# Performance work log

Measured on AMD Instinct MI355X. Metric: run time of the kernel, lower is better.

## Reference

```python
import jax, jax.numpy as jnp
import numpy as np

N = 100000   # nodes
E = 1600000  # edges (avg degree 16)
D = 64       # feature dim
LN_EPS = 1e-5


def setup_inputs() -> dict:
    key = jax.random.key(0)
    ks = jax.random.split(key, 12)
    s = 1.0 / np.sqrt(D)
    x = jax.random.normal(ks[0], (N, D), dtype=jnp.float32)
    edge_index = jax.random.randint(ks[1], (2, E), 0, N, dtype=jnp.int32)
    routing_factor = jax.random.uniform(ks[2], (E,), dtype=jnp.float32)
    return {
        "x": x,
        "edge_index": edge_index,
        "routing_factor": routing_factor,
        "W_phys": jax.random.normal(ks[3], (D, D), dtype=jnp.float32) * s,
        "W_neur": jax.random.normal(ks[4], (D, D), dtype=jnp.float32) * s,
        "att_w": jax.random.normal(ks[5], (2 * D,), dtype=jnp.float32) * s,
        "channel_fusion": jnp.float32(0.5),
        "mlp_w1": jax.random.normal(ks[6], (2 * D, D), dtype=jnp.float32) * s,
        "mlp_b1": jnp.zeros((2 * D,), dtype=jnp.float32),
        "mlp_w2": jax.random.normal(ks[7], (D, 2 * D), dtype=jnp.float32) / np.sqrt(2 * D),
        "mlp_b2": jnp.zeros((D,), dtype=jnp.float32),
        "ln1_g": jnp.ones((D,), dtype=jnp.float32),
        "ln1_b": jnp.zeros((D,), dtype=jnp.float32),
        "ln2_g": jnp.ones((D,), dtype=jnp.float32),
        "ln2_b": jnp.zeros((D,), dtype=jnp.float32),
    }


def _layernorm(h, g, b):
    mu = jnp.mean(h, axis=-1, keepdims=True)
    var = jnp.var(h, axis=-1, keepdims=True)
    return (h - mu) * jax.lax.rsqrt(var + LN_EPS) * g + b


def reference(x, edge_index, routing_factor, W_phys, W_neur, att_w,
              channel_fusion, mlp_w1, mlp_b1, mlp_w2, mlp_b2,
              ln1_g, ln1_b, ln2_g, ln2_b):
    src, dst = edge_index[0], edge_index[1]
    x_src = x[src]  # [E, D]
    # att(cat([x_src, x_dst])) == x_src @ w[:D] + x_dst @ w[D:]
    att_scores = x_src @ att_w[:D] + x[dst] @ att_w[D:]  # [E]
    # segment softmax over destination nodes (equivalent to per-node loop)
    seg_max = jax.ops.segment_max(att_scores, dst, num_segments=N)
    e = jnp.exp(att_scores - seg_max[dst])
    denom = jax.ops.segment_sum(e, dst, num_segments=N)
    att = e / denom[dst]  # [E]
    # dual-channel messages (dropout inactive at eval)
    phys = routing_factor[:, None] * (x_src @ W_phys.T)
    neur = x_src @ W_neur.T
    alpha = jax.nn.sigmoid(channel_fusion)
    messages = att[:, None] * (alpha * phys + (1.0 - alpha) * neur)  # [E, D]
    out = jax.ops.segment_sum(messages, dst, num_segments=N)  # [N, D]
    h = _layernorm(jax.nn.gelu(out, approximate=False) + x, ln1_g, ln1_b)
    m = jax.nn.gelu(h @ mlp_w1.T + mlp_b1, approximate=False) @ mlp_w2.T + mlp_b2
    return _layernorm(m + h, ln2_g, ln2_b)
```

## Files before the change

### kernel.cpp

```cpp
#include <hip/hip_runtime.h>
#include <math.h>

#define NN 100000
#define NE 1600000
#define DD 64
#define NBUK 782
#define TILE 8192
#define NTB ((NE + TILE - 1) / TILE)
#define NWB 96
#define NPB ((NN + 255) / 256)
#define BSTRIDE 3072
#define SCAP 3072

typedef __attribute__((ext_vector_type(8))) short short8;
typedef __attribute__((ext_vector_type(4))) float f32x4;
typedef __attribute__((ext_vector_type(4))) _Float16 h4;
typedef __attribute__((ext_vector_type(2))) _Float16 f16x2;

__device__ __forceinline__ float gelu_exact(float v) {
    return 0.5f * v * (1.0f + erff(v * 0.7071067811865475f));
}

__device__ __forceinline__ unsigned short f2bf(float f) {
    unsigned u = __float_as_uint(f);
    return (unsigned short)((u + 0x7FFFu + ((u >> 16) & 1u)) >> 16);
}
__device__ __forceinline__ float bf2f(unsigned short h) {
    return __uint_as_float((unsigned)h << 16);
}
__device__ __forceinline__ void split8v(float4 x0, float4 x1, short8& hi, short8& lo) {
    float v[8] = {x0.x, x0.y, x0.z, x0.w, x1.x, x1.y, x1.z, x1.w};
    #pragma unroll
    for (int i = 0; i < 8; ++i) {
        unsigned short h = f2bf(v[i]);
        hi[i] = (short)h;
        lo[i] = (short)f2bf(v[i] - bf2f(h));
    }
}
__device__ __forceinline__ void lds_frag(const float* g, int row, int u0, int s,
                                         short8& hi, short8& lo) {
    float4 p0 = *(const float4*)&g[row * 64 + ((u0 ^ s) << 2)];
    float4 p1 = *(const float4*)&g[row * 64 + (((u0 + 1) ^ s) << 2)];
    split8v(p0, p1, hi, lo);
}

__device__ __forceinline__ f16x2 as_f16x2(unsigned int u) {
    union { unsigned int x; f16x2 h; } c; c.x = u; return c.h;
}
__device__ __forceinline__ unsigned short h_as_us(_Float16 h) {
    union { _Float16 h; unsigned short u; } c; c.h = h; return c.u;
}
__device__ __forceinline__ float us_as_f(unsigned short u) {
    union { unsigned short u; _Float16 h; } c; c.u = u; return (float)c.h;
}

__global__ __launch_bounds__(256) void kfront(
    const int* __restrict__ ei, const float* __restrict__ rf,
    int* __restrict__ bcount, uint2* __restrict__ tmp,
    const float* __restrict__ Wp, const float* __restrict__ Wn,
    const float* __restrict__ w1, const float* __restrict__ w2,
    const float* __restrict__ cf,
    unsigned short* __restrict__ wh, unsigned short* __restrict__ wl,
    const float* __restrict__ x, const float* __restrict__ attw,
    float* __restrict__ es1, _Float16* __restrict__ xh)
{
    __shared__ int hist[NBUK];
    __shared__ int gbase[NBUK];
    int bid = blockIdx.x;
    int tid = threadIdx.x;

    if (bid < NTB) {
        for (int i = tid; i < NBUK; i += 256) hist[i] = 0;
        __syncthreads();
        int base = bid * TILE;
        int end  = min(base + TILE, NE);
        for (int e = base + tid; e < end; e += 256)
            atomicAdd(&hist[ei[NE + e] >> 7], 1);
        __syncthreads();
        for (int i = tid; i < NBUK; i += 256) {
            int c = hist[i];
            gbase[i] = c ? (i * BSTRIDE + atomicAdd(bcount + i, c)) : 0;
            hist[i] = 0;
        }
        __syncthreads();
        for (int e0 = base + tid; e0 < end; e0 += 256 * 4) {
            int srcs[4], dsts[4]; unsigned rfs[4];
            #pragma unroll
            for (int q = 0; q < 4; ++q) {
                int e = e0 + q * 256;
                if (e < end) {
                    srcs[q] = ei[e];
                    dsts[q] = ei[NE + e];
                    rfs[q]  = __float_as_uint(rf[e]);
                }
            }
            #pragma unroll
            for (int q = 0; q < 4; ++q) {
                int e = e0 + q * 256;
                if (e < end) {
                    int b = dsts[q] >> 7;
                    int t = atomicAdd(&hist[b], 1);
                    tmp[gbase[b] + t] = make_uint2(
                        (unsigned)srcs[q] | ((unsigned)(dsts[q] & 127) << 17),
                        rfs[q]);
                }
            }
        }
    } else if (bid < NTB + NWB) {
        int t = (bid - NTB) * 256 + tid;
        float alpha = 1.0f / (1.0f + __expf(-cf[0]));
        float beta  = 1.0f - alpha;
        float v;
        if (t < 8192) {
            int d = t >> 7, k = t & 127;
            v = (k < 64) ? alpha * Wp[d * 64 + k] : beta * Wn[d * 64 + (k - 64)];
        } else if (t < 16384) {
            v = w1[t - 8192];
        } else {
            v = w2[t - 16384];
        }
        unsigned short h = f2bf(v);
        wh[t] = h;
        wl[t] = f2bf(v - bf2f(h));
    } else {
        int n = (bid - NTB - NWB) * 256 + tid;
        if (n >= NN) return;
        const float4* x4 = (const float4*)(x + (size_t)n * DD);
        float a = 0.f;
        #pragma unroll
        for (int i = 0; i < DD/4; ++i) {
            float4 v = x4[i];
            a += v.x*attw[4*i+0] + v.y*attw[4*i+1] + v.z*attw[4*i+2] + v.w*attw[4*i+3];
            h4 hv = {(_Float16)v.x, (_Float16)v.y, (_Float16)v.z, (_Float16)v.w};
            *(h4*)(xh + (size_t)n * DD + 4*i) = hv;
        }
        es1[n] = __expf(a);
    }
}

__global__ __launch_bounds__(1024) void ks_bscan(
    const int* __restrict__ bcount, int* __restrict__ bbase)
{
    __shared__ int sa[1024], sb[1024];
    int t = threadIdx.x;
    int v = (t < NBUK) ? bcount[t] : 0;
    sa[t] = v;
    __syncthreads();
    int* s = sa; int* d = sb;
    #pragma unroll
    for (int o = 1; o < 1024; o <<= 1) {
        d[t] = s[t] + ((t >= o) ? s[t - o] : 0);
        __syncthreads();
        int* tmp = s; s = d; d = tmp;
    }
    if (t < NBUK) bbase[t] = s[t] - v;
    if (t == 0) bbase[NBUK] = NE;
}

__global__ __launch_bounds__(256) void kscat2(
    const uint2* __restrict__ tmp, const int* __restrict__ bcount,
    const int* __restrict__ bbase, const float* __restrict__ es1,
    int* __restrict__ off, uint2* __restrict__ sorted)
{
    __shared__ int hist[128], scn[128], tick[128];
    __shared__ uint2 obuf[SCAP];
    int b   = blockIdx.x;
    int tid = threadIdx.x;
    int si = b * BSTRIDE;
    int so = bbase[b];
    int m  = bcount[b];

    if (tid < 128) { hist[tid] = 0; tick[tid] = 0; }
    __syncthreads();

    for (int i = tid; i < m; i += 256)
        atomicAdd(&hist[tmp[si + i].x >> 17], 1);
    __syncthreads();

    if (tid < 128) scn[tid] = hist[tid];
    __syncthreads();
    #pragma unroll
    for (int o = 1; o < 128; o <<= 1) {
        int v = (tid < 128 && tid >= o) ? scn[tid - o] : 0;
        __syncthreads();
        if (tid < 128) scn[tid] += v;
        __syncthreads();
    }

    int nb0 = b * 128;
    if (tid < 128 && nb0 + tid < NN) off[nb0 + tid] = so + scn[tid] - hist[tid];
    if (b == NBUK - 1 && tid == 0) off[NN] = NE;
    __syncthreads();

    for (int i = tid; i < m; i += 256) {
        uint2 pr = tmp[si + i];
        int l   = pr.x >> 17;
        int src = pr.x & 0x1FFFF;
        float es = es1[src];
        float ef = es * __uint_as_float(pr.y);
        unsigned packed = (unsigned)h_as_us((_Float16)es)
                        | ((unsigned)h_as_us((_Float16)ef) << 16);
        int t = atomicAdd(&tick[l], 1);
        int lp = (scn[l] - hist[l]) + t;
        uint2 val = make_uint2((unsigned)src, packed);
        if (lp < SCAP) obuf[lp] = val;
        else sorted[so + lp] = val;
    }
    __syncthreads();
    int mm = min(m, SCAP);
    for (int i = tid; i < mm; i += 256)
        sorted[so + i] = obuf[i];
}

__global__ __launch_bounds__(256) void k4a_agg(
    const uint2* __restrict__ sorted, const int* __restrict__ off,
    const _Float16* __restrict__ xh, float* __restrict__ uv)
{
    int lane = threadIdx.x & 63;
    int n = blockIdx.x * 4 + (threadIdx.x >> 6);
    int r0 = __builtin_amdgcn_readfirstlane(off[n]);
    int r1 = __builtin_amdgcn_readfirstlane(off[n + 1]);
    const unsigned short* xs = (const unsigned short*)xh;

    float den = 0.f, u = 0.f, v = 0.f;
    const unsigned ONES = 0x3C003C00u;
    int j = r0;
    for (; j + 8 <= r1; j += 8) {
        uint2 p[8];
        #pragma unroll
        for (int t = 0; t < 8; ++t) p[t] = sorted[j + t];
        unsigned xv[4];
        #pragma unroll
        for (int q = 0; q < 4; ++q) {
            unsigned a0 = xs[(size_t)p[2*q].x   * DD + lane];
            unsigned a1 = xs[(size_t)p[2*q+1].x * DD + lane];
            xv[q] = a0 | (a1 << 16);
        }
        #pragma unroll
        for (int q = 0; q < 4; ++q) {
            unsigned y0 = p[2*q].y, y1 = p[2*q+1].y;
            unsigned e2 = (y0 & 0xFFFFu) | (y1 << 16);
            unsigned f2 = (y0 >> 16) | (y1 & 0xFFFF0000u);
            v   = __builtin_amdgcn_fdot2(as_f16x2(xv[q]), as_f16x2(e2), v, false);
            u   = __builtin_amdgcn_fdot2(as_f16x2(xv[q]), as_f16x2(f2), u, false);
            den = __builtin_amdgcn_fdot2(as_f16x2(e2), as_f16x2(ONES), den, false);
        }
    }
    for (; j + 2 <= r1; j += 2) {
        uint2 p0 = sorted[j], p1 = sorted[j + 1];
        unsigned a0 = xs[(size_t)p0.x * DD + lane];
        unsigned a1 = xs[(size_t)p1.x * DD + lane];
        unsigned xv = a0 | (a1 << 16);
        unsigned e2 = (p0.y & 0xFFFFu) | (p1.y << 16);
        unsigned f2 = (p0.y >> 16) | (p1.y & 0xFFFF0000u);
        v   = __builtin_amdgcn_fdot2(as_f16x2(xv), as_f16x2(e2), v, false);
        u   = __builtin_amdgcn_fdot2(as_f16x2(xv), as_f16x2(f2), u, false);
        den = __builtin_amdgcn_fdot2(as_f16x2(e2), as_f16x2(ONES), den, false);
    }
    if (j < r1) {
        uint2 p0 = sorted[j];
        float xvf = us_as_f((unsigned short)xs[(size_t)p0.x * DD + lane]);
        float e = us_as_f((unsigned short)(p0.y & 0xFFFFu));
        float f = us_as_f((unsigned short)(p0.y >> 16));
        den += e; v += e * xvf; u += f * xvf;
    }
    float inv = (r1 > r0) ? 1.f / den : 0.f;
    uv[(size_t)n * 128 + lane]      = u * inv;
    uv[(size_t)n * 128 + 64 + lane] = v * inv;
}

__global__ __launch_bounds__(512, 4) void k4b5(
    const float* __restrict__ uv,
    const unsigned short* __restrict__ wh, const unsigned short* __restrict__ wl,
    const float* __restrict__ x,
    const float* __restrict__ g1, const float* __restrict__ be1,
    const float* __restrict__ bb1, const float* __restrict__ bb2,
    const float* __restrict__ g2, const float* __restrict__ be2,
    float* __restrict__ out)
{
    __shared__ unsigned short WH[8192], WL[8192];
    __shared__ unsigned short W2H[4096], W2L[4096];
    __shared__ float Gt[8][1024];

    int tid  = threadIdx.x;
    int lane = tid & 63;
    int wv   = tid >> 6;
    int quad = lane >> 4, l16 = lane & 15;
    int s7   = l16 & 7;
    int nb = blockIdx.x * 128 + wv * 16;
    float* gt = Gt[wv];

    const float4* arow4 = (const float4*)(uv + (size_t)min(nb + l16, NN - 1) * 128);
    float4 av[8];
    #pragma unroll
    for (int ks = 0; ks < 4; ++ks) {
        av[2*ks]   = arow4[ks*8 + quad*2];
        av[2*ks+1] = arow4[ks*8 + quad*2 + 1];
    }
    float xr[4][4];
    #pragma unroll
    for (int r = 0; r < 4; ++r) {
        size_t nld = (size_t)min(nb + quad*4 + r, NN - 1) * 64;
        #pragma unroll
        for (int nt = 0; nt < 4; ++nt) xr[r][nt] = x[nld + nt*16 + l16];
    }

    #pragma unroll
    for (int k = 0; k < 2; ++k) {
        int i = tid + k*512;
        int row = i >> 4, u = i & 15;
        int up = u ^ (row & 7);
        *(short8*)&WH[row*128 + up*8] = *(const short8*)&wh[i*8];
        *(short8*)&WL[row*128 + up*8] = *(const short8*)&wl[i*8];
    }
    __syncthreads();

    f32x4 acc0[4] = {};
    #pragma unroll
    for (int ks = 0; ks < 4; ++ks) {
        short8 ah, al;
        split8v(av[2*ks], av[2*ks+1], ah, al);
        int u0 = 4*ks + quad;
        #pragma unroll
        for (int nt = 0; nt < 4; ++nt) {
            int wo = (nt*16 + l16)*128 + (u0 ^ s7)*8;
            short8 bh = *(const short8*)&WH[wo];
            short8 bl = *(const short8*)&WL[wo];
            acc0[nt] = __builtin_amdgcn_mfma_f32_16x16x32_bf16(ah, bh, acc0[nt], 0, 0, 0);
            acc0[nt] = __builtin_amdgcn_mfma_f32_16x16x32_bf16(al, bh, acc0[nt], 0, 0, 0);
            acc0[nt] = __builtin_amdgcn_mfma_f32_16x16x32_bf16(ah, bl, acc0[nt], 0, 0, 0);
        }
    }

    float hn[4][4];
    #pragma unroll
    for (int r = 0; r < 4; ++r) {
        float hv[4];
        #pragma unroll
        for (int nt = 0; nt < 4; ++nt)
            hv[nt] = gelu_exact(acc0[nt][r]) + xr[r][nt];
        float s = hv[0] + hv[1] + hv[2] + hv[3];
        #pragma unroll
        for (int o = 1; o < 16; o <<= 1) s += __shfl_xor(s, o);
        float mu = s * (1.0f/64.0f);
        float q = 0.f;
        #pragma unroll
        for (int nt = 0; nt < 4; ++nt) { float t = hv[nt] - mu; q += t*t; }
        #pragma unroll
        for (int o = 1; o < 16; o <<= 1) q += __shfl_xor(q, o);
        float rs = rsqrtf(q * (1.0f/64.0f) + 1e-5f);
        int row = quad*4 + r;
        #pragma unroll
        for (int nt = 0; nt < 4; ++nt) {
            int c = nt*16 + l16;
            float h = (hv[nt] - mu) * rs * g1[c] + be1[c];
            hn[r][nt] = h;
            int u = c >> 2;
            gt[row*64 + ((u ^ (row & 7)) << 2) + (c & 3)] = h;
        }
    }
    __syncthreads();

    #pragma unroll
    for (int k = 0; k < 2; ++k) {
        int i = tid + k*512;
        int row = i >> 3, u = i & 7;
        int up = u ^ (row & 7);
        *(short8*)&WH[row*64 + up*8] = *(const short8*)&wh[8192 + i*8];
        *(short8*)&WL[row*64 + up*8] = *(const short8*)&wl[8192 + i*8];
    }
    {
        int row = tid >> 3, u = tid & 7;
        int up = u ^ (row & 7);
        *(short8*)&W2H[row*64 + up*8] = *(const short8*)&wh[16384 + row*128 + u*8];
        *(short8*)&W2L[row*64 + up*8] = *(const short8*)&wl[16384 + row*128 + u*8];
    }
    __syncthreads();

    short8 ah1[2], al1[2];
    #pragma unroll
    for (int ks = 0; ks < 2; ++ks)
        lds_frag(gt, l16, 8*ks + 2*quad, s7, ah1[ks], al1[ks]);

    f32x4 acc2[4] = {};
    #pragma unroll
    for (int half = 0; half < 2; ++half) {
        f32x4 a1[4] = {};
        #pragma unroll
        for (int ks = 0; ks < 2; ++ks) {
            int u0 = 4*ks + quad;
            #pragma unroll
            for (int t = 0; t < 4; ++t) {
                int row = half*64 + t*16 + l16;
                int wo = row*64 + ((u0 ^ s7))*8;
                short8 bh = *(const short8*)&WH[wo];
                short8 bl = *(const short8*)&WL[wo];
                a1[t] = __builtin_amdgcn_mfma_f32_16x16x32_bf16(ah1[ks], bh, a1[t], 0, 0, 0);
                a1[t] = __builtin_amdgcn_mfma_f32_16x16x32_bf16(al1[ks], bh, a1[t], 0, 0, 0);
                a1[t] = __builtin_amdgcn_mfma_f32_16x16x32_bf16(ah1[ks], bl, a1[t], 0, 0, 0);
            }
        }
        #pragma unroll
        for (int t = 0; t < 4; ++t) {
            float b1v = bb1[half*64 + t*16 + l16];
            #pragma unroll
            for (int r = 0; r < 4; ++r) {
                int row = quad*4 + r;
                int c = t*16 + l16;
                int u = c >> 2;
                gt[row*64 + ((u ^ (row & 7)) << 2) + (c & 3)] = gelu_exact(a1[t][r] + b1v);
            }
        }
        #pragma unroll
        for (int ks2 = 0; ks2 < 2; ++ks2) {
            short8 ah2, al2;
            lds_frag(gt, l16, 8*ks2 + 2*quad, s7, ah2, al2);
            int u0 = 4*ks2 + quad;
            #pragma unroll
            for (int nt2 = 0; nt2 < 4; ++nt2) {
                int wo = (nt2*16 + l16)*64 + (u0 ^ s7)*8;
                short8 bh = *(const short8*)&W2H[wo];
                short8 bl = *(const short8*)&W2L[wo];
                acc2[nt2] = __builtin_amdgcn_mfma_f32_16x16x32_bf16(ah2, bh, acc2[nt2], 0, 0, 0);
                acc2[nt2] = __builtin_amdgcn_mfma_f32_16x16x32_bf16(al2, bh, acc2[nt2], 0, 0, 0);
                acc2[nt2] = __builtin_amdgcn_mfma_f32_16x16x32_bf16(ah2, bl, acc2[nt2], 0, 0, 0);
            }
        }
        if (half == 0) {
            __syncthreads();
            int row = tid >> 3, u = tid & 7;
            int up = u ^ (row & 7);
            *(short8*)&W2H[row*64 + up*8] = *(const short8*)&wh[16384 + row*128 + 64 + u*8];
            *(short8*)&W2L[row*64 + up*8] = *(const short8*)&wl[16384 + row*128 + 64 + u*8];
            __syncthreads();
        }
    }

    #pragma unroll
    for (int r = 0; r < 4; ++r) {
        int n = nb + quad * 4 + r;
        float mv[4];
        #pragma unroll
        for (int nt = 0; nt < 4; ++nt)
            mv[nt] = acc2[nt][r] + hn[r][nt] + bb2[nt*16 + l16];
        float s = mv[0] + mv[1] + mv[2] + mv[3];
        #pragma unroll
        for (int o = 1; o < 16; o <<= 1) s += __shfl_xor(s, o);
        float mu = s * (1.0f/64.0f);
        float q = 0.f;
        #pragma unroll
        for (int nt = 0; nt < 4; ++nt) { float t = mv[nt] - mu; q += t*t; }
        #pragma unroll
        for (int o = 1; o < 16; o <<= 1) q += __shfl_xor(q, o);
        float rs = rsqrtf(q * (1.0f/64.0f) + 1e-5f);
        if (n < NN) {
            #pragma unroll
            for (int nt = 0; nt < 4; ++nt) {
                int c = nt*16 + l16;
                out[(size_t)n * 64 + c] = (mv[nt] - mu) * rs * g2[c] + be2[c];
            }
        }
    }
}

extern "C" void kernel_launch(void* const* d_in, const int* in_sizes, int n_in,
                              void* d_out, int out_size, void* d_ws, size_t ws_size,
                              hipStream_t stream) {
    const float* x    = (const float*)d_in[0];
    const int*   ei   = (const int*)d_in[1];
    const float* rf   = (const float*)d_in[2];
    const float* Wp   = (const float*)d_in[3];
    const float* Wn   = (const float*)d_in[4];
    const float* attw = (const float*)d_in[5];
    const float* cf   = (const float*)d_in[6];
    const float* w1   = (const float*)d_in[7];
    const float* b1   = (const float*)d_in[8];
    const float* w2   = (const float*)d_in[9];
    const float* b2   = (const float*)d_in[10];
    const float* g1   = (const float*)d_in[11];
    const float* be1  = (const float*)d_in[12];
    const float* g2   = (const float*)d_in[13];
    const float* be2  = (const float*)d_in[14];
    float* out = (float*)d_out;

    float* ws = (float*)d_ws;
    float*  es1    = ws;
    float*  uv     = es1 + NN;
    unsigned short* wh = (unsigned short*)(uv + (size_t)NN * 128);
    unsigned short* wl = wh + 24576;
    uint2*  sorted = (uint2*)(wl + 24576);
    int*    off    = (int*)(sorted + NE);
    int*    bcount = off + NN + 1;
    int*    bbase  = bcount + NBUK;
    uintptr_t xp = ((uintptr_t)(bbase + NBUK + 1) + 15) & ~(uintptr_t)15;
    _Float16* xh = (_Float16*)xp;
    uint2*  tmp    = (uint2*)uv;

    hipMemsetAsync(bcount, 0, NBUK * sizeof(int), stream);

    kfront    <<<NTB + NWB + NPB, 256, 0, stream>>>(ei, rf, bcount, tmp,
                 Wp, Wn, w1, w2, cf, wh, wl, x, attw, es1, xh);
    ks_bscan  <<<1, 1024, 0, stream>>>(bcount, bbase);
    kscat2    <<<NBUK, 256, 0, stream>>>(tmp, bcount, bbase, es1, off, sorted);
    k4a_agg   <<<NN/4, 256, 0, stream>>>(sorted, off, xh, uv);
    k4b5      <<<(NN+127)/128, 512, 0, stream>>>(uv, wh, wl, x, g1, be1, b1, b2, g2, be2, out);
}
```

Before: 263.3 us.

## Switch fused MLP kernel from split-bf16 to fp16 MFMA and fp16 intermediates

```diff
diff --git a/kernel.cpp b/kernel.cpp
--- a/kernel.cpp
+++ b/kernel.cpp
@@ -12,7 +12,7 @@
 #define BSTRIDE 3072
 #define SCAP 3072
 
-typedef __attribute__((ext_vector_type(8))) short short8;
+typedef __attribute__((ext_vector_type(8))) _Float16 half8;
 typedef __attribute__((ext_vector_type(4))) float f32x4;
 typedef __attribute__((ext_vector_type(4))) _Float16 h4;
 typedef __attribute__((ext_vector_type(2))) _Float16 f16x2;
@@ -21,29 +21,6 @@
     return 0.5f * v * (1.0f + erff(v * 0.7071067811865475f));
 }
 
-__device__ __forceinline__ unsigned short f2bf(float f) {
-    unsigned u = __float_as_uint(f);
-    return (unsigned short)((u + 0x7FFFu + ((u >> 16) & 1u)) >> 16);
-}
-__device__ __forceinline__ float bf2f(unsigned short h) {
-    return __uint_as_float((unsigned)h << 16);
-}
-__device__ __forceinline__ void split8v(float4 x0, float4 x1, short8& hi, short8& lo) {
-    float v[8] = {x0.x, x0.y, x0.z, x0.w, x1.x, x1.y, x1.z, x1.w};
-    #pragma unroll
-    for (int i = 0; i < 8; ++i) {
-        unsigned short h = f2bf(v[i]);
-        hi[i] = (short)h;
-        lo[i] = (short)f2bf(v[i] - bf2f(h));
-    }
-}
-__device__ __forceinline__ void lds_frag(const float* g, int row, int u0, int s,
-                                         short8& hi, short8& lo) {
-    float4 p0 = *(const float4*)&g[row * 64 + ((u0 ^ s) << 2)];
-    float4 p1 = *(const float4*)&g[row * 64 + (((u0 + 1) ^ s) << 2)];
-    split8v(p0, p1, hi, lo);
-}
-
 __device__ __forceinline__ f16x2 as_f16x2(unsigned int u) {
     union { unsigned int x; f16x2 h; } c; c.x = u; return c.h;
 }
@@ -53,6 +30,8 @@
 __device__ __forceinline__ float us_as_f(unsigned short u) {
     union { unsigned short u; _Float16 h; } c; c.u = u; return (float)c.h;
 }
+
+#define BFRAG(W, row, u0) (*(const half8*)&W[(row)*64 + ((((u0) ^ ((row)&7)))<<3)])
 
 __global__ __launch_bounds__(256) void kfront(
     const int* __restrict__ ei, const float* __restrict__ rf,
@@ -60,7 +39,7 @@
     const float* __restrict__ Wp, const float* __restrict__ Wn,
     const float* __restrict__ w1, const float* __restrict__ w2,
     const float* __restrict__ cf,
-    unsigned short* __restrict__ wh, unsigned short* __restrict__ wl,
+    _Float16* __restrict__ whh, _Float16* __restrict__ wll,
     const float* __restrict__ x, const float* __restrict__ attw,
     float* __restrict__ es1, _Float16* __restrict__ xh)
 {
@@ -119,9 +98,9 @@
         } else {
             v = w2[t - 16384];
         }
-        unsigned short h = f2bf(v);
-        wh[t] = h;
-        wl[t] = f2bf(v - bf2f(h));
+        _Float16 h = (_Float16)v;
+        whh[t] = h;
+        wll[t] = (_Float16)(v - (float)h);
     } else {
         int n = (bid - NTB - NWB) * 256 + tid;
         if (n >= NN) return;
@@ -214,7 +193,7 @@
 
 __global__ __launch_bounds__(256) void k4a_agg(
     const uint2* __restrict__ sorted, const int* __restrict__ off,
-    const _Float16* __restrict__ xh, float* __restrict__ uv)
+    const _Float16* __restrict__ xh, _Float16* __restrict__ uvh)
 {
     int lane = threadIdx.x & 63;
     int n = blockIdx.x * 4 + (threadIdx.x >> 6);
@@ -265,38 +244,35 @@
         den += e; v += e * xvf; u += f * xvf;
     }
     float inv = (r1 > r0) ? 1.f / den : 0.f;
-    uv[(size_t)n * 128 + lane]      = u * inv;
-    uv[(size_t)n * 128 + 64 + lane] = v * inv;
-}
-
-__global__ __launch_bounds__(512, 4) void k4b5(
-    const float* __restrict__ uv,
-    const unsigned short* __restrict__ wh, const unsigned short* __restrict__ wl,
+    uvh[(size_t)n * 128 + lane]      = (_Float16)(u * inv);
+    uvh[(size_t)n * 128 + 64 + lane] = (_Float16)(v * inv);
+}
+
+__global__ __launch_bounds__(512, 6) void k4b5(
+    const _Float16* __restrict__ uvh,
+    const _Float16* __restrict__ whh, const _Float16* __restrict__ wll,
     const float* __restrict__ x,
     const float* __restrict__ g1, const float* __restrict__ be1,
     const float* __restrict__ bb1, const float* __restrict__ bb2,
     const float* __restrict__ g2, const float* __restrict__ be2,
     float* __restrict__ out)
 {
-    __shared__ unsigned short WH[8192], WL[8192];
-    __shared__ unsigned short W2H[4096], W2L[4096];
-    __shared__ float Gt[8][1024];
+    __shared__ _Float16 WAH[4096], WAL[4096];
+    __shared__ _Float16 W2H[4096], W2L[4096];
+    __shared__ _Float16 Gt[8][1024];
 
     int tid  = threadIdx.x;
     int lane = tid & 63;
     int wv   = tid >> 6;
     int quad = lane >> 4, l16 = lane & 15;
-    int s7   = l16 & 7;
     int nb = blockIdx.x * 128 + wv * 16;
-    float* gt = Gt[wv];
-
-    const float4* arow4 = (const float4*)(uv + (size_t)min(nb + l16, NN - 1) * 128);
-    float4 av[8];
-    #pragma unroll
-    for (int ks = 0; ks < 4; ++ks) {
-        av[2*ks]   = arow4[ks*8 + quad*2];
-        av[2*ks+1] = arow4[ks*8 + quad*2 + 1];
-    }
+    _Float16* gt = Gt[wv];
+
+    const _Float16* arow = uvh + (size_t)min(nb + l16, NN - 1) * 128;
+    half8 av[4];
+    #pragma unroll
+    for (int ks = 0; ks < 4; ++ks)
+        av[ks] = *(const half8*)(arow + ks*32 + quad*8);
     float xr[4][4];
     #pragma unroll
     for (int r = 0; r < 4; ++r) {
@@ -305,30 +281,39 @@
         for (int nt = 0; nt < 4; ++nt) xr[r][nt] = x[nld + nt*16 + l16];
     }
 
-    #pragma unroll
-    for (int k = 0; k < 2; ++k) {
-        int i = tid + k*512;
-        int row = i >> 4, u = i & 15;
-        int up = u ^ (row & 7);
-        *(short8*)&WH[row*128 + up*8] = *(const short8*)&wh[i*8];
-        *(short8*)&WL[row*128 + up*8] = *(const short8*)&wl[i*8];
-    }
+    int srow = tid >> 3, su = tid & 7;
+    int sdst = srow*64 + ((su ^ (srow & 7)) << 3);
+
+    *(half8*)&WAH[sdst] = *(const half8*)&whh[srow*128 + su*8];
+    *(half8*)&WAL[sdst] = *(const half8*)&wll[srow*128 + su*8];
+    *(half8*)&W2H[sdst] = *(const half8*)&whh[16384 + srow*128 + su*8];
+    *(half8*)&W2L[sdst] = *(const half8*)&wll[16384 + srow*128 + su*8];
     __syncthreads();
 
     f32x4 acc0[4] = {};
     #pragma unroll
-    for (int ks = 0; ks < 4; ++ks) {
-        short8 ah, al;
-        split8v(av[2*ks], av[2*ks+1], ah, al);
-        int u0 = 4*ks + quad;
+    for (int ks = 0; ks < 2; ++ks) {
+        int u0 = ks*4 + quad;
         #pragma unroll
         for (int nt = 0; nt < 4; ++nt) {
-            int wo = (nt*16 + l16)*128 + (u0 ^ s7)*8;
-            short8 bh = *(const short8*)&WH[wo];
-            short8 bl = *(const short8*)&WL[wo];
-            acc0[nt] = __builtin_amdgcn_mfma_f32_16x16x32_bf16(ah, bh, acc0[nt], 0, 0, 0);
-            acc0[nt] = __builtin_amdgcn_mfma_f32_16x16x32_bf16(al, bh, acc0[nt], 0, 0, 0);
-            acc0[nt] = __builtin_amdgcn_mfma_f32_16x16x32_bf16(ah, bl, acc0[nt], 0, 0, 0);
+            int row = nt*16 + l16;
+            acc0[nt] = __builtin_amdgcn_mfma_f32_16x16x32_f16(av[ks], BFRAG(WAH,row,u0), acc0[nt], 0,0,0);
+            acc0[nt] = __builtin_amdgcn_mfma_f32_16x16x32_f16(av[ks], BFRAG(WAL,row,u0), acc0[nt], 0,0,0);
+        }
+    }
+    __syncthreads();
+    *(half8*)&WAH[sdst] = *(const half8*)&whh[srow*128 + 64 + su*8];
+    *(half8*)&WAL[sdst] = *(const half8*)&wll[srow*128 + 64 + su*8];
+    __syncthreads();
+
+    #pragma unroll
+    for (int ks = 0; ks < 2; ++ks) {
+        int u0 = ks*4 + quad;
+        #pragma unroll
+        for (int nt = 0; nt < 4; ++nt) {
+            int row = nt*16 + l16;
+            acc0[nt] = __builtin_amdgcn_mfma_f32_16x16x32_f16(av[2+ks], BFRAG(WAH,row,u0), acc0[nt], 0,0,0);
+            acc0[nt] = __builtin_amdgcn_mfma_f32_16x16x32_f16(av[2+ks], BFRAG(WAL,row,u0), acc0[nt], 0,0,0);
         }
     }
 
@@ -355,84 +340,98 @@
             int c = nt*16 + l16;
             float h = (hv[nt] - mu) * rs * g1[c] + be1[c];
             hn[r][nt] = h;
-            int u = c >> 2;
-            gt[row*64 + ((u ^ (row & 7)) << 2) + (c & 3)] = h;
-        }
-    }
-    __syncthreads();
-
-    #pragma unroll
-    for (int k = 0; k < 2; ++k) {
-        int i = tid + k*512;
-        int row = i >> 3, u = i & 7;
-        int up = u ^ (row & 7);
-        *(short8*)&WH[row*64 + up*8] = *(const short8*)&wh[8192 + i*8];
-        *(short8*)&WL[row*64 + up*8] = *(const short8*)&wl[8192 + i*8];
-    }
+            int u = c >> 3;
+            gt[row*64 + ((u ^ (row & 7)) << 3) + (c & 7)] = (_Float16)h;
+        }
+    }
+    half8 ah1[2];
+    #pragma unroll
+    for (int ks = 0; ks < 2; ++ks) {
+        int u0 = ks*4 + quad;
+        ah1[ks] = *(const half8*)&gt[l16*64 + ((u0 ^ (l16 & 7)) << 3)];
+    }
+    __syncthreads();
+    *(half8*)&WAH[sdst] = *(const half8*)&whh[8192 + srow*64 + su*8];
+    *(half8*)&WAL[sdst] = *(const half8*)&wll[8192 + srow*64 + su*8];
+    __syncthreads();
+
+    f32x4 acc2[4] = {};
     {
-        int row = tid >> 3, u = tid & 7;
-        int up = u ^ (row & 7);
-        *(short8*)&W2H[row*64 + up*8] = *(const short8*)&wh[16384 + row*128 + u*8];
-        *(short8*)&W2L[row*64 + up*8] = *(const short8*)&wl[16384 + row*128 + u*8];
-    }
-    __syncthreads();
-
-    short8 ah1[2], al1[2];
-    #pragma unroll
-    for (int ks = 0; ks < 2; ++ks)
-        lds_frag(gt, l16, 8*ks + 2*quad, s7, ah1[ks], al1[ks]);
-
-    f32x4 acc2[4] = {};
-    #pragma unroll
-    for (int half = 0; half < 2; ++half) {
         f32x4 a1[4] = {};
         #pragma unroll
         for (int ks = 0; ks < 2; ++ks) {
-            int u0 = 4*ks + quad;
+            int u0 = ks*4 + quad;
             #pragma unroll
             for (int t = 0; t < 4; ++t) {
-                int row = half*64 + t*16 + l16;
-                int wo = row*64 + ((u0 ^ s7))*8;
-                short8 bh = *(const short8*)&WH[wo];
-                short8 bl = *(const short8*)&WL[wo];
-                a1[t] = __builtin_amdgcn_mfma_f32_16x16x32_bf16(ah1[ks], bh, a1[t], 0, 0, 0);
-                a1[t] = __builtin_amdgcn_mfma_f32_16x16x32_bf16(al1[ks], bh, a1[t], 0, 0, 0);
-                a1[t] = __builtin_amdgcn_mfma_f32_16x16x32_bf16(ah1[ks], bl, a1[t], 0, 0, 0);
+                int row = t*16 + l16;
+                a1[t] = __builtin_amdgcn_mfma_f32_16x16x32_f16(ah1[ks], BFRAG(WAH,row,u0), a1[t], 0,0,0);
+                a1[t] = __builtin_amdgcn_mfma_f32_16x16x32_f16(ah1[ks], BFRAG(WAL,row,u0), a1[t], 0,0,0);
             }
         }
         #pragma unroll
         for (int t = 0; t < 4; ++t) {
-            float b1v = bb1[half*64 + t*16 + l16];
+            float b1v = bb1[t*16 + l16];
             #pragma unroll
             for (int r = 0; r < 4; ++r) {
                 int row = quad*4 + r;
                 int c = t*16 + l16;
-                int u = c >> 2;
-                gt[row*64 + ((u ^ (row & 7)) << 2) + (c & 3)] = gelu_exact(a1[t][r] + b1v);
+                int u = c >> 3;
+                gt[row*64 + ((u ^ (row & 7)) << 3) + (c & 7)] =
+                    (_Float16)gelu_exact(a1[t][r] + b1v);
             }
         }
         #pragma unroll
         for (int ks2 = 0; ks2 < 2; ++ks2) {
-            short8 ah2, al2;
-            lds_frag(gt, l16, 8*ks2 + 2*quad, s7, ah2, al2);
-            int u0 = 4*ks2 + quad;
+            int u0 = ks2*4 + quad;
+            half8 ag = *(const half8*)&gt[l16*64 + ((u0 ^ (l16 & 7)) << 3)];
             #pragma unroll
             for (int nt2 = 0; nt2 < 4; ++nt2) {
-                int wo = (nt2*16 + l16)*64 + (u0 ^ s7)*8;
-                short8 bh = *(const short8*)&W2H[wo];
-                short8 bl = *(const short8*)&W2L[wo];
-                acc2[nt2] = __builtin_amdgcn_mfma_f32_16x16x32_bf16(ah2, bh, acc2[nt2], 0, 0, 0);
-                acc2[nt2] = __builtin_amdgcn_mfma_f32_16x16x32_bf16(al2, bh, acc2[nt2], 0, 0, 0);
-                acc2[nt2] = __builtin_amdgcn_mfma_f32_16x16x32_bf16(ah2, bl, acc2[nt2], 0, 0, 0);
-            }
-        }
-        if (half == 0) {
-            __syncthreads();
-            int row = tid >> 3, u = tid & 7;
-            int up = u ^ (row & 7);
-            *(short8*)&W2H[row*64 + up*8] = *(const short8*)&wh[16384 + row*128 + 64 + u*8];
-            *(short8*)&W2L[row*64 + up*8] = *(const short8*)&wl[16384 + row*128 + 64 + u*8];
-            __syncthreads();
+                int row = nt2*16 + l16;
+                acc2[nt2] = __builtin_amdgcn_mfma_f32_16x16x32_f16(ag, BFRAG(W2H,row,u0), acc2[nt2], 0,0,0);
+                acc2[nt2] = __builtin_amdgcn_mfma_f32_16x16x32_f16(ag, BFRAG(W2L,row,u0), acc2[nt2], 0,0,0);
+            }
+        }
+    }
+    __syncthreads();
+    *(half8*)&WAH[sdst] = *(const half8*)&whh[8192 + (64 + srow)*64 + su*8];
+    *(half8*)&WAL[sdst] = *(const half8*)&wll[8192 + (64 + srow)*64 + su*8];
+    *(half8*)&W2H[sdst] = *(const half8*)&whh[16384 + srow*128 + 64 + su*8];
+    *(half8*)&W2L[sdst] = *(const half8*)&wll[16384 + srow*128 + 64 + su*8];
+    __syncthreads();
+    {
+        f32x4 a1[4] = {};
+        #pragma unroll
+        for (int ks = 0; ks < 2; ++ks) {
+            int u0 = ks*4 + quad;
+            #pragma unroll
+            for (int t = 0; t < 4; ++t) {
+                int row = t*16 + l16;
+                a1[t] = __builtin_amdgcn_mfma_f32_16x16x32_f16(ah1[ks], BFRAG(WAH,row,u0), a1[t], 0,0,0);
+                a1[t] = __builtin_amdgcn_mfma_f32_16x16x32_f16(ah1[ks], BFRAG(WAL,row,u0), a1[t], 0,0,0);
+            }
+        }
+        #pragma unroll
+        for (int t = 0; t < 4; ++t) {
+            float b1v = bb1[64 + t*16 + l16];
+            #pragma unroll
+            for (int r = 0; r < 4; ++r) {
+                int row = quad*4 + r;
+                int c = t*16 + l16;
+                int u = c >> 3;
+                gt[row*64 + ((u ^ (row & 7)) << 3) + (c & 7)] =
+                    (_Float16)gelu_exact(a1[t][r] + b1v);
+            }
+        }
+        #pragma unroll
+        for (int ks2 = 0; ks2 < 2; ++ks2) {
+            int u0 = ks2*4 + quad;
+            half8 ag = *(const half8*)&gt[l16*64 + ((u0 ^ (l16 & 7)) << 3)];
+            #pragma unroll
+            for (int nt2 = 0; nt2 < 4; ++nt2) {
+                int row = nt2*16 + l16;
+                acc2[nt2] = __builtin_amdgcn_mfma_f32_16x16x32_f16(ag, BFRAG(W2H,row,u0), acc2[nt2], 0,0,0);
+                acc2[nt2] = __builtin_amdgcn_mfma_f32_16x16x32_f16(ag, BFRAG(W2L,row,u0), acc2[nt2], 0,0,0);
+            }
         }
     }
 
@@ -484,24 +483,24 @@
     float* out = (float*)d_out;
 
     float* ws = (float*)d_ws;
-    float*  es1    = ws;
-    float*  uv     = es1 + NN;
-    unsigned short* wh = (unsigned short*)(uv + (size_t)NN * 128);
-    unsigned short* wl = wh + 24576;
-    uint2*  sorted = (uint2*)(wl + 24576);
+    float*     es1 = ws;
+    _Float16*  uvh = (_Float16*)(es1 + NN);
+    _Float16*  whh = uvh + (size_t)NN * 128;
+    _Float16*  wll = whh + 24576;
+    uint2*  sorted = (uint2*)(wll + 24576);
     int*    off    = (int*)(sorted + NE);
     int*    bcount = off + NN + 1;
     int*    bbase  = bcount + NBUK;
     uintptr_t xp = ((uintptr_t)(bbase + NBUK + 1) + 15) & ~(uintptr_t)15;
     _Float16* xh = (_Float16*)xp;
-    uint2*  tmp    = (uint2*)uv;
+    uint2*  tmp    = (uint2*)uvh;
 
     hipMemsetAsync(bcount, 0, NBUK * sizeof(int), stream);
 
     kfront    <<<NTB + NWB + NPB, 256, 0, stream>>>(ei, rf, bcount, tmp,
-                 Wp, Wn, w1, w2, cf, wh, wl, x, attw, es1, xh);
+                 Wp, Wn, w1, w2, cf, whh, wll, x, attw, es1, xh);
     ks_bscan  <<<1, 1024, 0, stream>>>(bcount, bbase);
     kscat2    <<<NBUK, 256, 0, stream>>>(tmp, bcount, bbase, es1, off, sorted);
-    k4a_agg   <<<NN/4, 256, 0, stream>>>(sorted, off, xh, uv);
-    k4b5      <<<(NN+127)/128, 512, 0, stream>>>(uv, wh, wl, x, g1, be1, b1, b2, g2, be2, out);
-}
+    k4a_agg   <<<NN/4, 256, 0, stream>>>(sorted, off, xh, uvh);
+    k4b5      <<<(NN+127)/128, 512, 0, stream>>>(uvh, whh, wll, x, g1, be1, b1, b2, g2, be2, out);
+}
```

Result: slower. 280.0 us (+6.4%).
